# Kernel optimization log

Hardware: AMD Instinct MI355X
Metric: run time of the kernel (lower is better)

## Reference

```python
import jax, jax.numpy as jnp
import numpy as np

B, K, NPER, Fin, Fmem, H = 64, 16, 256, 256, 128, 8
LN_EPS = 1e-5


def _build_edges():
    # each memory slot (src) attends over all K slots + NPER nodes of its batch elem
    BK = B * K
    dest_chunks = []
    for b in range(B):
        dest_b = np.concatenate([b * K + np.arange(K), BK + b * NPER + np.arange(NPER)])
        dest_chunks.append(np.tile(dest_b, K))
    dest = np.concatenate(dest_chunks).astype(np.int32)
    src = np.repeat(np.arange(BK), K + NPER).astype(np.int32)
    return src, dest


def setup_inputs() -> dict:
    key = jax.random.key(0)
    ks = jax.random.split(key, 16)
    N = B * NPER
    BK = B * K
    src, dest = _build_edges()
    s = 0.02
    return {
        'x': jax.random.normal(ks[0], (N, Fin), jnp.float32),
        'memory': jax.random.normal(ks[1], (BK, Fmem), jnp.float32),
        'Wp': jax.random.normal(ks[2], (Fin, Fmem), jnp.float32) * s,
        'bp': jnp.zeros((Fmem,), jnp.float32),
        'Wqkv': jax.random.normal(ks[3], (Fmem, 3 * Fmem), jnp.float32) * s,  # bias=False
        'ln1_g': jnp.ones((Fmem,), jnp.float32),
        'ln1_b': jnp.zeros((Fmem,), jnp.float32),
        'W1': jax.random.normal(ks[4], (Fmem, Fmem), jnp.float32) * s,
        'b1': jnp.zeros((Fmem,), jnp.float32),
        'W2': jax.random.normal(ks[5], (Fmem, Fmem), jnp.float32) * s,
        'b2': jnp.zeros((Fmem,), jnp.float32),
        'ln2_g': jnp.ones((Fmem,), jnp.float32),
        'ln2_b': jnp.zeros((Fmem,), jnp.float32),
        'Wg': jax.random.normal(ks[6], (2 * Fmem, 2 * Fmem), jnp.float32) * s,
        'bg': jnp.zeros((2 * Fmem,), jnp.float32),
        'src': jnp.asarray(src),
        'dest': jnp.asarray(dest),
    }


def layer_norm(x, g, b):
    mu = x.mean(-1, keepdims=True)
    var = ((x - mu) ** 2).mean(-1, keepdims=True)
    return (x - mu) * jax.lax.rsqrt(var + LN_EPS) * g + b


def reference(x, memory, Wp, bp, Wqkv, ln1_g, ln1_b, W1, b1, W2, b2,
              ln2_g, ln2_b, Wg, bg, src, dest):
    BK, F = memory.shape
    Fh = F // H
    # input projection and concat [memory; x]
    xp = x @ Wp + bp                               # [N, Fmem]
    mem_cat = jnp.concatenate([memory, xp], 0)     # [BK + N, Fmem]
    # qkv projection (no bias), Fqk = Fv = Fmem
    q, k, v = jnp.split(mem_cat @ Wqkv, 3, axis=-1)
    q = (q * (float(Fh) ** -0.5)).reshape(-1, H, Fh)
    k = k.reshape(-1, H, Fh)
    v = v.reshape(-1, H, Fh)
    # per-edge attention scores
    aw = jnp.einsum('ehf,ehf->eh', q[src], k[dest])          # [E, H]
    # scatter softmax over src segments
    m = jax.ops.segment_max(aw, src, num_segments=BK)
    e = jnp.exp(aw - m[src])
    z = jax.ops.segment_sum(e, src, num_segments=BK)
    p = e / z[src]                                            # [E, H]
    # weighted scatter-sum aggregation
    out = jax.ops.segment_sum(p[:, :, None] * v[dest], src, num_segments=BK)
    out = out.reshape(BK, F)
    # residual + LN, MLP, residual + LN
    mem_tmp = layer_norm(memory + out, ln1_g, ln1_b)
    mem_update = jax.nn.relu(mem_tmp @ W1 + b1) @ W2 + b2
    mem_update = layer_norm(mem_tmp + mem_update, ln2_g, ln2_b)
    # feature-level LSTM-style gating
    gate = jnp.concatenate([memory, mem_update], -1) @ Wg + bg
    f, i = jnp.split(gate, 2, axis=-1)
    new_mem = memory * jax.nn.sigmoid(f) + mem_update * jax.nn.sigmoid(i)
    return new_mem  # original returns (output, memory) with output is memory
```

## Files before the change

kernel.cpp:

```cpp
#include <hip/hip_runtime.h>
#include <hip/hip_bf16.h>

#define B_    64
#define K_    16
#define NPER_ 256
#define FIN_  256
#define F_    128
#define H_    8
#define N_    (B_ * NPER_)
#define BK_   (B_ * K_)
#define KV_   (K_ + NPER_)
#define LN_EPS_ 1e-5f

typedef short short8v __attribute__((ext_vector_type(8)));
typedef float float4v __attribute__((ext_vector_type(4)));

__device__ __forceinline__ float bf2f(unsigned short u) {
    union { unsigned u; float f; } c; c.u = ((unsigned)u) << 16; return c.f;
}
template<bool BF>
__device__ __forceinline__ float ldT(const void* p, long i) {
    if (BF) return bf2f(((const unsigned short*)p)[i]);
    else    return ((const float*)p)[i];
}
template<bool BF>
__device__ __forceinline__ float2 ld2T(const void* p, long i) {
    if (BF) {
        const unsigned u = *(const unsigned*)((const unsigned short*)p + i);
        return make_float2(bf2f((unsigned short)(u & 0xffffu)),
                           bf2f((unsigned short)(u >> 16)));
    } else {
        return *(const float2*)((const float*)p + i);
    }
}
template<bool BF>
__device__ __forceinline__ float4 ld4T(const void* p, long i) {
    if (BF) {
        const uint2 u = *(const uint2*)((const unsigned short*)p + i);
        return make_float4(bf2f((unsigned short)(u.x & 0xffffu)),
                           bf2f((unsigned short)(u.x >> 16)),
                           bf2f((unsigned short)(u.y & 0xffffu)),
                           bf2f((unsigned short)(u.y >> 16)));
    } else {
        return *(const float4*)((const float*)p + i);
    }
}
template<bool BF>
__device__ __forceinline__ void stT(void* p, long i, float v) {
    if (BF) ((__hip_bfloat16*)p)[i] = __float2bfloat16(v);
    else    ((float*)p)[i] = v;
}
__device__ __forceinline__ bool is_bf(const unsigned* probe) {
    return probe[0] != 0x3F800000u;
}

__device__ __forceinline__ unsigned short f2bf_rne(float f) {
    union { float f; unsigned u; } c; c.f = f;
    const unsigned r = c.u + 0x7FFFu + ((c.u >> 16) & 1u);
    return (unsigned short)(r >> 16);
}
__device__ __forceinline__ unsigned long long pack4(unsigned short a, unsigned short b,
                                                    unsigned short c, unsigned short d) {
    return (unsigned long long)a | ((unsigned long long)b << 16)
         | ((unsigned long long)c << 32) | ((unsigned long long)d << 48);
}

#define LDK 40

template<bool BF>
__device__ void gemm_xp_body(const void* x, const void* Wp, const void* bp,
                             float* xp, short* Ah, short* Al, short* Bh, short* Bl) {
    const int t = threadIdx.x;
    const int row0 = blockIdx.x * 32;
    const int wave = t >> 6, lane = t & 63;
    const int wm = wave >> 1, wn = wave & 1;
    const int l15 = lane & 15, l4 = lane >> 4;
    float4v acc[4];
    #pragma unroll
    for (int fc = 0; fc < 4; ++fc) acc[fc] = (float4v){0.f, 0.f, 0.f, 0.f};

    for (int ks = 0; ks < 8; ++ks) {
        const int k0 = ks * 32;
        {
            const int ar = t >> 3, kq = (t & 7) * 4;
            const float4 v4 = ld4T<BF>(x, (long)(row0 + ar) * FIN_ + k0 + kq);
            unsigned short h0 = f2bf_rne(v4.x), h1 = f2bf_rne(v4.y);
            unsigned short h2 = f2bf_rne(v4.z), h3 = f2bf_rne(v4.w);
            *(unsigned long long*)(Ah + ar * LDK + kq) = pack4(h0, h1, h2, h3);
            *(unsigned long long*)(Al + ar * LDK + kq) = pack4(
                f2bf_rne(v4.x - bf2f(h0)), f2bf_rne(v4.y - bf2f(h1)),
                f2bf_rne(v4.z - bf2f(h2)), f2bf_rne(v4.w - bf2f(h3)));
        }
        {
            const int j = t & 127, khh = (t >> 7) * 16;
            unsigned short hh[16], ll[16];
            #pragma unroll
            for (int kk = 0; kk < 16; ++kk) {
                const float w = ldT<BF>(Wp, (long)(k0 + khh + kk) * F_ + j);
                hh[kk] = f2bf_rne(w);
                ll[kk] = f2bf_rne(w - bf2f(hh[kk]));
            }
            #pragma unroll
            for (int g = 0; g < 4; ++g) {
                *(unsigned long long*)(Bh + j * LDK + khh + 4 * g) =
                    pack4(hh[4*g], hh[4*g+1], hh[4*g+2], hh[4*g+3]);
                *(unsigned long long*)(Bl + j * LDK + khh + 4 * g) =
                    pack4(ll[4*g], ll[4*g+1], ll[4*g+2], ll[4*g+3]);
            }
        }
        __syncthreads();
        {
            const int abase = (wm * 16 + l15) * LDK + 8 * l4;
            const short8v ah = *(const short8v*)(Ah + abase);
            const short8v al = *(const short8v*)(Al + abase);
            #pragma unroll
            for (int fc = 0; fc < 4; ++fc) {
                const int bbase = (wn * 64 + fc * 16 + l15) * LDK + 8 * l4;
                const short8v bh = *(const short8v*)(Bh + bbase);
                const short8v bl = *(const short8v*)(Bl + bbase);
                acc[fc] = __builtin_amdgcn_mfma_f32_16x16x32_bf16(ah, bh, acc[fc], 0, 0, 0);
                acc[fc] = __builtin_amdgcn_mfma_f32_16x16x32_bf16(ah, bl, acc[fc], 0, 0, 0);
                acc[fc] = __builtin_amdgcn_mfma_f32_16x16x32_bf16(al, bh, acc[fc], 0, 0, 0);
            }
        }
        __syncthreads();
    }
    #pragma unroll
    for (int fc = 0; fc < 4; ++fc) {
        const int col = wn * 64 + fc * 16 + l15;
        const float bb = ldT<BF>(bp, col);
        #pragma unroll
        for (int reg = 0; reg < 4; ++reg) {
            const int row = row0 + wm * 16 + l4 * 4 + reg;
            xp[(long)row * F_ + col] = acc[fc][reg] + bb;
        }
    }
}
__global__ __launch_bounds__(256) void k_gemm_xp(const void* x, const void* Wp,
        const void* bp, const unsigned* probe, float* xp) {
    __shared__ __align__(16) short Ah[32 * LDK];
    __shared__ __align__(16) short Al[32 * LDK];
    __shared__ __align__(16) short Bh[128 * LDK];
    __shared__ __align__(16) short Bl[128 * LDK];
    if (is_bf(probe)) gemm_xp_body<true >(x, Wp, bp, xp, Ah, Al, Bh, Bl);
    else              gemm_xp_body<false>(x, Wp, bp, xp, Ah, Al, Bh, Bl);
}

template<bool BF>
__device__ void gemm_qkv_body(const float* xp, const void* mem, const void* Wqkv,
                              float* kx, float* vx, float* qm, float* km, float* vm,
                              short* Ah, short* Al, short* Bh, short* Bl) {
    const int mb = blockIdx.x, nb = blockIdx.y;
    const bool isMem = (mb >= 512);
    const int t = threadIdx.x;
    const int wave = t >> 6, lane = t & 63;
    const int wm = wave >> 1, wn = wave & 1;
    const int l15 = lane & 15, l4 = lane >> 4;
    float4v acc[4];
    #pragma unroll
    for (int fc = 0; fc < 4; ++fc) acc[fc] = (float4v){0.f, 0.f, 0.f, 0.f};

    for (int ks = 0; ks < 4; ++ks) {
        const int k0 = ks * 32;
        {
            const int ar = t >> 3, kq = (t & 7) * 4;
            float4 v4;
            if (isMem) v4 = ld4T<BF>(mem, (long)((mb - 512) * 32 + ar) * F_ + k0 + kq);
            else       v4 = *(const float4*)(xp + (long)(mb * 32 + ar) * F_ + k0 + kq);
            unsigned short h0 = f2bf_rne(v4.x), h1 = f2bf_rne(v4.y);
            unsigned short h2 = f2bf_rne(v4.z), h3 = f2bf_rne(v4.w);
            *(unsigned long long*)(Ah + ar * LDK + kq) = pack4(h0, h1, h2, h3);
            *(unsigned long long*)(Al + ar * LDK + kq) = pack4(
                f2bf_rne(v4.x - bf2f(h0)), f2bf_rne(v4.y - bf2f(h1)),
                f2bf_rne(v4.z - bf2f(h2)), f2bf_rne(v4.w - bf2f(h3)));
        }
        {
            const int j = t & 127, khh = (t >> 7) * 16;
            unsigned short hh[16], ll[16];
            #pragma unroll
            for (int kk = 0; kk < 16; ++kk) {
                const float w = ldT<BF>(Wqkv, (long)(k0 + khh + kk) * 384 + nb * 128 + j);
                hh[kk] = f2bf_rne(w);
                ll[kk] = f2bf_rne(w - bf2f(hh[kk]));
            }
            #pragma unroll
            for (int g = 0; g < 4; ++g) {
                *(unsigned long long*)(Bh + j * LDK + khh + 4 * g) =
                    pack4(hh[4*g], hh[4*g+1], hh[4*g+2], hh[4*g+3]);
                *(unsigned long long*)(Bl + j * LDK + khh + 4 * g) =
                    pack4(ll[4*g], ll[4*g+1], ll[4*g+2], ll[4*g+3]);
            }
        }
        __syncthreads();
        {
            const int abase = (wm * 16 + l15) * LDK + 8 * l4;
            const short8v ah = *(const short8v*)(Ah + abase);
            const short8v al = *(const short8v*)(Al + abase);
            #pragma unroll
            for (int fc = 0; fc < 4; ++fc) {
                const int bbase = (wn * 64 + fc * 16 + l15) * LDK + 8 * l4;
                const short8v bh = *(const short8v*)(Bh + bbase);
                const short8v bl = *(const short8v*)(Bl + bbase);
                acc[fc] = __builtin_amdgcn_mfma_f32_16x16x32_bf16(ah, bh, acc[fc], 0, 0, 0);
                acc[fc] = __builtin_amdgcn_mfma_f32_16x16x32_bf16(ah, bl, acc[fc], 0, 0, 0);
                acc[fc] = __builtin_amdgcn_mfma_f32_16x16x32_bf16(al, bh, acc[fc], 0, 0, 0);
            }
        }
        __syncthreads();
    }
    #pragma unroll
    for (int fc = 0; fc < 4; ++fc) {
        const int col = wn * 64 + fc * 16 + l15;
        #pragma unroll
        for (int reg = 0; reg < 4; ++reg) {
            const int mrow = mb * 32 + wm * 16 + l4 * 4 + reg;
            const float v = acc[fc][reg];
            if (!isMem) {
                ((nb == 1) ? kx : vx)[(long)mrow * F_ + col] = v;
            } else {
                const long s = mrow - 16384;
                if      (nb == 0) qm[s * F_ + col] = v * 0.25f;
                else if (nb == 1) km[s * F_ + col] = v;
                else              vm[s * F_ + col] = v;
            }
        }
    }
}
__global__ __launch_bounds__(256) void k_gemm_qkv(const float* xp, const void* mem,
        const void* Wqkv, const unsigned* probe,
        float* kx, float* vx, float* qm, float* km, float* vm) {
    if (blockIdx.y == 0 && blockIdx.x < 512) return;
    __shared__ __align__(16) short Ah[32 * LDK];
    __shared__ __align__(16) short Al[32 * LDK];
    __shared__ __align__(16) short Bh[128 * LDK];
    __shared__ __align__(16) short Bl[128 * LDK];
    if (is_bf(probe)) gemm_qkv_body<true >(xp, mem, Wqkv, kx, vx, qm, km, vm, Ah, Al, Bh, Bl);
    else              gemm_qkv_body<false>(xp, mem, Wqkv, kx, vx, qm, km, vm, Ah, Al, Bh, Bl);
}

#define KPAD 20
__global__ __launch_bounds__(256) void k_attn(const float* qm, const float* km,
        const float* vm, const float* kx, const float* vx, float* attn_out) {
    __shared__ float qh[16 * 16];
    __shared__ float kh[KV_ * KPAD];
    __shared__ float vh[KV_ * KPAD];
    __shared__ float S[16 * KV_];
    const int b = blockIdx.x >> 3, h = blockIdx.x & 7;
    const int t = threadIdx.x;
    qh[t] = qm[(long)(b * 16 + (t >> 4)) * F_ + h * 16 + (t & 15)];
    if (t < 64) {
        const int e = t >> 2, d4 = (t & 3) * 4;
        const long a = (long)(b * K_ + e) * F_ + h * 16 + d4;
        *(float4*)(kh + e * KPAD + d4) = *(const float4*)(km + a);
        *(float4*)(vh + e * KPAD + d4) = *(const float4*)(vm + a);
    }
    #pragma unroll
    for (int p = 0; p < 4; ++p) {
        const int i = t + p * 256;
        const int e = i >> 2, d4 = (i & 3) * 4;
        const long a = ((long)(b * NPER_) + e) * F_ + h * 16 + d4;
        *(float4*)(kh + (16 + e) * KPAD + d4) = *(const float4*)(kx + a);
        *(float4*)(vh + (16 + e) * KPAD + d4) = *(const float4*)(vx + a);
    }
    __syncthreads();
    {
        const int e = t;
        float acc[16];
        #pragma unroll
        for (int r = 0; r < 16; ++r) acc[r] = 0.f;
        #pragma unroll
        for (int dq = 0; dq < 16; dq += 4) {
            const float4 k4 = *(const float4*)(kh + e * KPAD + dq);
            #pragma unroll
            for (int r = 0; r < 16; ++r) {
                const float4 q4 = *(const float4*)(qh + r * 16 + dq);
                acc[r] += q4.x * k4.x + q4.y * k4.y + q4.z * k4.z + q4.w * k4.w;
            }
        }
        #pragma unroll
        for (int r = 0; r < 16; ++r) S[r * KV_ + e] = acc[r];
        const int e2 = 256 + (t >> 4), r2 = t & 15;
        float a2 = 0.f;
        #pragma unroll
        for (int dq = 0; dq < 16; dq += 4) {
            const float4 k4 = *(const float4*)(kh + e2 * KPAD + dq);
            const float4 q4 = *(const float4*)(qh + r2 * 16 + dq);
            a2 += q4.x * k4.x + q4.y * k4.y + q4.z * k4.z + q4.w * k4.w;
        }
        S[r2 * KV_ + e2] = a2;
    }
    __syncthreads();
    {
        const int wave = t >> 6, lane = t & 63;
        for (int r = wave; r < 16; r += 4) {
            float m = -1e30f;
            for (int e = lane; e < KV_; e += 64) m = fmaxf(m, S[r * KV_ + e]);
            for (int off = 32; off; off >>= 1) m = fmaxf(m, __shfl_xor(m, off));
            float z = 0.f;
            for (int e = lane; e < KV_; e += 64) {
                const float p = __expf(S[r * KV_ + e] - m);
                S[r * KV_ + e] = p; z += p;
            }
            for (int off = 32; off; off >>= 1) z += __shfl_xor(z, off);
            const float inv = 1.f / z;
            for (int e = lane; e < KV_; e += 64) S[r * KV_ + e] *= inv;
        }
    }
    __syncthreads();
    {
        const int r = t >> 4, d = t & 15;
        float o0 = 0.f, o1 = 0.f, o2 = 0.f, o3 = 0.f;
        for (int e = 0; e < KV_; e += 4) {
            const float4 p4 = *(const float4*)(S + r * KV_ + e);
            o0 += p4.x * vh[(e + 0) * KPAD + d];
            o1 += p4.y * vh[(e + 1) * KPAD + d];
            o2 += p4.z * vh[(e + 2) * KPAD + d];
            o3 += p4.w * vh[(e + 3) * KPAD + d];
        }
        attn_out[((long)(b * 16) + r) * F_ + h * 16 + d] = (o0 + o1) + (o2 + o3);
    }
}

#define R4 2
template<bool BF>
__device__ void post_body(const void* mem, const float* attn,
                          const void* ln1g, const void* ln1b,
                          const void* W1, const void* b1,
                          const void* W2, const void* b2,
                          const void* ln2g, const void* ln2b,
                          const void* Wg, const void* bg,
                          void* out,
                          float* ms, float* hs, float* ts, float* cat,
                          float* gs, float (*pb)[R4][256]) {
    const int t = threadIdx.x;
    const int r0b = blockIdx.x * R4;
    if (t < 128) {
        const int rr = t >> 6, c0 = (t & 63) * 2;
        const long gbase = (long)(r0b + rr) * F_ + c0;
        const float mv0 = ldT<BF>(mem, gbase), mv1 = ldT<BF>(mem, gbase + 1);
        const float2 a2 = *(const float2*)(attn + gbase);
        const float y0 = mv0 + a2.x, y1 = mv1 + a2.y;
        float s = y0 + y1;
        #pragma unroll
        for (int off = 32; off; off >>= 1) s += __shfl_xor(s, off);
        const float mu = s * (1.f / 128.f);
        const float d0 = y0 - mu, d1 = y1 - mu;
        float v = d0 * d0 + d1 * d1;
        #pragma unroll
        for (int off = 32; off; off >>= 1) v += __shfl_xor(v, off);
        const float inv = rsqrtf(v * (1.f / 128.f) + LN_EPS_);
        ms[rr * F_ + c0]     = d0 * inv * ldT<BF>(ln1g, c0)     + ldT<BF>(ln1b, c0);
        ms[rr * F_ + c0 + 1] = d1 * inv * ldT<BF>(ln1g, c0 + 1) + ldT<BF>(ln1b, c0 + 1);
        cat[rr * 256 + c0]     = mv0;
        cat[rr * 256 + c0 + 1] = mv1;
    }
    __syncthreads();
    {
        const int jp2 = (t & 63) * 2, r = (t >> 6) & 1, kh = t >> 7;
        const float* mr = ms + r * F_ + kh * 64;
        float a0 = 0.f, a1 = 0.f, b0v = 0.f, b1v = 0.f;
        #pragma unroll 4
        for (int f = 0; f < 64; f += 4) {
            const float4 m4 = *(const float4*)(mr + f);
            const float2 w0 = ld2T<BF>(W1, (long)(kh * 64 + f + 0) * F_ + jp2);
            const float2 w1 = ld2T<BF>(W1, (long)(kh * 64 + f + 1) * F_ + jp2);
            const float2 w2 = ld2T<BF>(W1, (long)(kh * 64 + f + 2) * F_ + jp2);
            const float2 w3 = ld2T<BF>(W1, (long)(kh * 64 + f + 3) * F_ + jp2);
            a0  += m4.x * w0.x + m4.z * w2.x;
            a1  += m4.y * w1.x + m4.w * w3.x;
            b0v += m4.x * w0.y + m4.z * w2.y;
            b1v += m4.y * w1.y + m4.w * w3.y;
        }
        pb[kh][r][jp2]     = a0 + a1;
        pb[kh][r][jp2 + 1] = b0v + b1v;
    }
    __syncthreads();
    {
        const int r = t >> 7, c = t & 127;
        hs[r * F_ + c] = fmaxf(pb[0][r][c] + pb[1][r][c] + ldT<BF>(b1, c), 0.f);
    }
    __syncthreads();
    {
        const int jp2 = (t & 63) * 2, r = (t >> 6) & 1, kh = t >> 7;
        const float* hr = hs + r * F_ + kh * 64;
        float a0 = 0.f, a1 = 0.f, b0v = 0.f, b1v = 0.f;
        #pragma unroll 4
        for (int f = 0; f < 64; f += 4) {
            const float4 h4 = *(const float4*)(hr + f);
            const float2 w0 = ld2T<BF>(W2, (long)(kh * 64 + f + 0) * F_ + jp2);
            const float2 w1 = ld2T<BF>(W2, (long)(kh * 64 + f + 1) * F_ + jp2);
            const float2 w2 = ld2T<BF>(W2, (long)(kh * 64 + f + 2) * F_ + jp2);
            const float2 w3 = ld2T<BF>(W2, (long)(kh * 64 + f + 3) * F_ + jp2);
            a0  += h4.x * w0.x + h4.z * w2.x;
            a1  += h4.y * w1.x + h4.w * w3.x;
            b0v += h4.x * w0.y + h4.z * w2.y;
            b1v += h4.y * w1.y + h4.w * w3.y;
        }
        pb[kh][r][jp2]     = a0 + a1;
        pb[kh][r][jp2 + 1] = b0v + b1v;
    }
    __syncthreads();
    {
        const int r = t >> 7, c = t & 127;
        ts[r * F_ + c] = ms[r * F_ + c] + pb[0][r][c] + pb[1][r][c] + ldT<BF>(b2, c);
    }
    __syncthreads();
    if (t < 128) {
        const int rr = t >> 6, c0 = (t & 63) * 2;
        const float z0 = ts[rr * F_ + c0], z1 = ts[rr * F_ + c0 + 1];
        float s = z0 + z1;
        #pragma unroll
        for (int off = 32; off; off >>= 1) s += __shfl_xor(s, off);
        const float mu = s * (1.f / 128.f);
        const float d0 = z0 - mu, d1 = z1 - mu;
        float v = d0 * d0 + d1 * d1;
        #pragma unroll
        for (int off = 32; off; off >>= 1) v += __shfl_xor(v, off);
        const float inv = rsqrtf(v * (1.f / 128.f) + LN_EPS_);
        cat[rr * 256 + 128 + c0]     = d0 * inv * ldT<BF>(ln2g, c0)     + ldT<BF>(ln2b, c0);
        cat[rr * 256 + 128 + c0 + 1] = d1 * inv * ldT<BF>(ln2g, c0 + 1) + ldT<BF>(ln2b, c0 + 1);
    }
    __syncthreads();
    {
        const int cq4 = (t & 63) * 4, r = (t >> 6) & 1, kh = t >> 7;
        const float* cr = cat + r * 256 + kh * 128;
        float a0 = 0.f, a1 = 0.f, a2 = 0.f, a3 = 0.f;
        #pragma unroll 2
        for (int f = 0; f < 128; f += 4) {
            const float4 c4 = *(const float4*)(cr + f);
            float4 w;
            w = ld4T<BF>(Wg, (long)(kh * 128 + f + 0) * 256 + cq4);
            a0 += c4.x * w.x; a1 += c4.x * w.y; a2 += c4.x * w.z; a3 += c4.x * w.w;
            w = ld4T<BF>(Wg, (long)(kh * 128 + f + 1) * 256 + cq4);
            a0 += c4.y * w.x; a1 += c4.y * w.y; a2 += c4.y * w.z; a3 += c4.y * w.w;
            w = ld4T<BF>(Wg, (long)(kh * 128 + f + 2) * 256 + cq4);
            a0 += c4.z * w.x; a1 += c4.z * w.y; a2 += c4.z * w.z; a3 += c4.z * w.w;
            w = ld4T<BF>(Wg, (long)(kh * 128 + f + 3) * 256 + cq4);
            a0 += c4.w * w.x; a1 += c4.w * w.y; a2 += c4.w * w.z; a3 += c4.w * w.w;
        }
        pb[kh][r][cq4 + 0] = a0; pb[kh][r][cq4 + 1] = a1;
        pb[kh][r][cq4 + 2] = a2; pb[kh][r][cq4 + 3] = a3;
    }
    __syncthreads();
    {
        #pragma unroll
        for (int o = t; o < 512; o += 256) {
            const int r = o >> 8, c = o & 255;
            gs[r * 256 + c] = pb[0][r][c] + pb[1][r][c] + ldT<BF>(bg, c);
        }
    }
    __syncthreads();
    {
        const int r = t >> 7, cf = t & 127;
        const float gf = gs[r * 256 + cf], gi = gs[r * 256 + 128 + cf];
        const float m0 = cat[r * 256 + cf], uu = cat[r * 256 + 128 + cf];
        const float val = m0 * (1.f / (1.f + __expf(-gf)))
                        + uu * (1.f / (1.f + __expf(-gi)));
        stT<BF>(out, (long)(r0b + r) * F_ + cf, val);
    }
}
__global__ __launch_bounds__(256) void k_post(const void* mem, const float* attn,
        const void* ln1g, const void* ln1b, const void* W1, const void* b1,
        const void* W2, const void* b2, const void* ln2g, const void* ln2b,
        const void* Wg, const void* bg, const unsigned* probe, void* out) {
    __shared__ float ms[R4 * F_];
    __shared__ float hs[R4 * F_];
    __shared__ float ts[R4 * F_];
    __shared__ float cat[R4 * 2 * F_];
    __shared__ float gs[R4 * 2 * F_];
    __shared__ float pb[2][R4][256];
    if (is_bf(probe)) post_body<true >(mem, attn, ln1g, ln1b, W1, b1, W2, b2,
                                       ln2g, ln2b, Wg, bg, out, ms, hs, ts, cat, gs, pb);
    else              post_body<false>(mem, attn, ln1g, ln1b, W1, b1, W2, b2,
                                       ln2g, ln2b, Wg, bg, out, ms, hs, ts, cat, gs, pb);
}

extern "C" void kernel_launch(void* const* d_in, const int* in_sizes, int n_in,
                              void* d_out, int out_size, void* d_ws, size_t ws_size,
                              hipStream_t stream) {
    const void* x      = d_in[0];
    const void* memory = d_in[1];
    const void* Wp     = d_in[2];
    const void* bp     = d_in[3];
    const void* Wqkv   = d_in[4];
    const void* ln1g   = d_in[5];
    const void* ln1b   = d_in[6];
    const void* W1     = d_in[7];
    const void* b1     = d_in[8];
    const void* W2     = d_in[9];
    const void* b2     = d_in[10];
    const void* ln2g   = d_in[11];
    const void* ln2b   = d_in[12];
    const void* Wg     = d_in[13];
    const void* bg     = d_in[14];
    const unsigned* probe = (const unsigned*)d_in[5];

    float* ws   = (float*)d_ws;
    float* xp   = ws;
    float* kx   = xp + (long)N_ * F_;
    float* vx   = kx + (long)N_ * F_;
    float* qm   = vx + (long)N_ * F_;
    float* km   = qm + (long)BK_ * F_;
    float* vm   = km + (long)BK_ * F_;
    float* attn = vm + (long)BK_ * F_;

    k_gemm_xp  <<<N_ / 32, 256, 0, stream>>>(x, Wp, bp, probe, xp);
    k_gemm_qkv <<<dim3((N_ + BK_) / 32, 3), 256, 0, stream>>>(xp, memory, Wqkv, probe,
                                                              kx, vx, qm, km, vm);
    k_attn     <<<B_ * H_, 256, 0, stream>>>(qm, km, vm, kx, vx, attn);
    k_post     <<<BK_ / R4, 256, 0, stream>>>(memory, attn, ln1g, ln1b, W1, b1,
                                              W2, b2, ln2g, ln2b, Wg, bg, probe, d_out);
}
```

Measured before the change: 155.0 us.

## Fuse input projection and QKV GEMMs into one kernel keeping xp in LDS

Merges the x@Wp projection and the K/V projection of the node rows into one kernel. The projected tile stays in shared memory as a split bf16 hi/lo pair and is never written to global memory. Memory rows compute Q, K and V in the same launch. When inputs are bf16, the hi/lo split and the extra MFMAs are dropped for already-bf16 operands. This removes a launch and the xp global round trip, at the cost of larger LDS use (60KB) and lower occupancy per block.

```diff
diff --git a/kernel.cpp b/kernel.cpp
--- a/kernel.cpp
+++ b/kernel.cpp
@@ -66,176 +66,250 @@
 }
 
 #define LDK 40
+#define CH  (32 * LDK)
 
 template<bool BF>
-__device__ void gemm_xp_body(const void* x, const void* Wp, const void* bp,
-                             float* xp, short* Ah, short* Al, short* Bh, short* Bl) {
+__device__ void proj_body(const void* x, const void* mem, const void* Wp,
+                          const void* bp, const void* Wqkv,
+                          float* kx, float* vx, float* qm, float* km, float* vm,
+                          short* pool) {
     const int t = threadIdx.x;
-    const int row0 = blockIdx.x * 32;
+    const int mb = blockIdx.x;
     const int wave = t >> 6, lane = t & 63;
     const int wm = wave >> 1, wn = wave & 1;
     const int l15 = lane & 15, l4 = lane >> 4;
-    float4v acc[4];
-    #pragma unroll
-    for (int fc = 0; fc < 4; ++fc) acc[fc] = (float4v){0.f, 0.f, 0.f, 0.f};
-
-    for (int ks = 0; ks < 8; ++ks) {
-        const int k0 = ks * 32;
+    short* A2h = pool;
+    short* A2l = pool + 5120;
+    short* Rb  = pool + 10240;
+
+    if (mb < 512) {
+        const long row0 = (long)mb * 32;
+        short* A1h = Rb;
+        short* A1l = Rb + 1280;
+        short* B1h = Rb + 2560;
+        short* B1l = Rb + 7680;
+        float4v acc1[4];
+        #pragma unroll
+        for (int fc = 0; fc < 4; ++fc) acc1[fc] = (float4v){0.f, 0.f, 0.f, 0.f};
+        for (int ks = 0; ks < 8; ++ks) {
+            const int k0 = ks * 32;
+            {
+                const int ar = t >> 3, kq = (t & 7) * 4;
+                const long idx = (row0 + ar) * FIN_ + k0 + kq;
+                if (BF) {
+                    const uint2 u = *(const uint2*)((const unsigned short*)x + idx);
+                    *(uint2*)(A1h + ar * LDK + kq) = u;
+                } else {
+                    const float4 v4 = *(const float4*)((const float*)x + idx);
+                    unsigned short h0 = f2bf_rne(v4.x), h1 = f2bf_rne(v4.y);
+                    unsigned short h2 = f2bf_rne(v4.z), h3 = f2bf_rne(v4.w);
+                    *(unsigned long long*)(A1h + ar * LDK + kq) = pack4(h0, h1, h2, h3);
+                    *(unsigned long long*)(A1l + ar * LDK + kq) = pack4(
+                        f2bf_rne(v4.x - bf2f(h0)), f2bf_rne(v4.y - bf2f(h1)),
+                        f2bf_rne(v4.z - bf2f(h2)), f2bf_rne(v4.w - bf2f(h3)));
+                }
+            }
+            {
+                const int j = t & 127, kh0 = (t >> 7) * 16;
+                #pragma unroll
+                for (int q = 0; q < 4; ++q) {
+                    if (BF) {
+                        const unsigned short* w = (const unsigned short*)Wp;
+                        const long r = (long)(k0 + kh0 + 4 * q) * F_ + j;
+                        *(unsigned long long*)(B1h + j * LDK + kh0 + 4 * q) =
+                            pack4(w[r], w[r + F_], w[r + 2 * F_], w[r + 3 * F_]);
+                    } else {
+                        const float* w = (const float*)Wp;
+                        const long r = (long)(k0 + kh0 + 4 * q) * F_ + j;
+                        const float w0 = w[r], w1 = w[r + F_], w2 = w[r + 2 * F_], w3 = w[r + 3 * F_];
+                        unsigned short h0 = f2bf_rne(w0), h1 = f2bf_rne(w1);
+                        unsigned short h2 = f2bf_rne(w2), h3 = f2bf_rne(w3);
+                        *(unsigned long long*)(B1h + j * LDK + kh0 + 4 * q) = pack4(h0, h1, h2, h3);
+                        *(unsigned long long*)(B1l + j * LDK + kh0 + 4 * q) = pack4(
+                            f2bf_rne(w0 - bf2f(h0)), f2bf_rne(w1 - bf2f(h1)),
+                            f2bf_rne(w2 - bf2f(h2)), f2bf_rne(w3 - bf2f(h3)));
+                    }
+                }
+            }
+            __syncthreads();
+            {
+                const int ab = (wm * 16 + l15) * LDK + 8 * l4;
+                const short8v ah = *(const short8v*)(A1h + ab);
+                short8v al;
+                if (!BF) al = *(const short8v*)(A1l + ab);
+                #pragma unroll
+                for (int fc = 0; fc < 4; ++fc) {
+                    const int bb = (wn * 64 + fc * 16 + l15) * LDK + 8 * l4;
+                    const short8v bh = *(const short8v*)(B1h + bb);
+                    acc1[fc] = __builtin_amdgcn_mfma_f32_16x16x32_bf16(ah, bh, acc1[fc], 0, 0, 0);
+                    if (!BF) {
+                        const short8v bl = *(const short8v*)(B1l + bb);
+                        acc1[fc] = __builtin_amdgcn_mfma_f32_16x16x32_bf16(ah, bl, acc1[fc], 0, 0, 0);
+                        acc1[fc] = __builtin_amdgcn_mfma_f32_16x16x32_bf16(al, bh, acc1[fc], 0, 0, 0);
+                    }
+                }
+            }
+            __syncthreads();
+        }
+        #pragma unroll
+        for (int fc = 0; fc < 4; ++fc) {
+            const int col = wn * 64 + fc * 16 + l15;
+            const int c = col >> 5, kk = col & 31;
+            const float bb = ldT<BF>(bp, col);
+            #pragma unroll
+            for (int reg = 0; reg < 4; ++reg) {
+                const int row = wm * 16 + l4 * 4 + reg;
+                const float v = acc1[fc][reg] + bb;
+                const unsigned short h = f2bf_rne(v);
+                A2h[c * CH + row * LDK + kk] = (short)h;
+                A2l[c * CH + row * LDK + kk] = (short)f2bf_rne(v - bf2f(h));
+            }
+        }
+        short* B2h = Rb;
+        short* B2l = Rb + 10240;
+        float4v acc2[8];
+        #pragma unroll
+        for (int fc = 0; fc < 8; ++fc) acc2[fc] = (float4v){0.f, 0.f, 0.f, 0.f};
+        for (int c2 = 0; c2 < 4; ++c2) {
+            __syncthreads();
+            {
+                const int jj = t;
+                #pragma unroll
+                for (int q = 0; q < 8; ++q) {
+                    const long r = (long)(c2 * 32 + 4 * q) * 384 + 128 + jj;
+                    if (BF) {
+                        const unsigned short* w = (const unsigned short*)Wqkv;
+                        *(unsigned long long*)(B2h + jj * LDK + 4 * q) =
+                            pack4(w[r], w[r + 384], w[r + 768], w[r + 1152]);
+                    } else {
+                        const float* w = (const float*)Wqkv;
+                        const float w0 = w[r], w1 = w[r + 384], w2 = w[r + 768], w3 = w[r + 1152];
+                        unsigned short h0 = f2bf_rne(w0), h1 = f2bf_rne(w1);
+                        unsigned short h2 = f2bf_rne(w2), h3 = f2bf_rne(w3);
+                        *(unsigned long long*)(B2h + jj * LDK + 4 * q) = pack4(h0, h1, h2, h3);
+                        *(unsigned long long*)(B2l + jj * LDK + 4 * q) = pack4(
+                            f2bf_rne(w0 - bf2f(h0)), f2bf_rne(w1 - bf2f(h1)),
+                            f2bf_rne(w2 - bf2f(h2)), f2bf_rne(w3 - bf2f(h3)));
+                    }
+                }
+            }
+            __syncthreads();
+            {
+                const int ab = c2 * CH + (wm * 16 + l15) * LDK + 8 * l4;
+                const short8v a2h = *(const short8v*)(A2h + ab);
+                const short8v a2l = *(const short8v*)(A2l + ab);
+                #pragma unroll
+                for (int fc = 0; fc < 8; ++fc) {
+                    const int bb = (wn * 128 + fc * 16 + l15) * LDK + 8 * l4;
+                    const short8v bh = *(const short8v*)(B2h + bb);
+                    acc2[fc] = __builtin_amdgcn_mfma_f32_16x16x32_bf16(a2h, bh, acc2[fc], 0, 0, 0);
+                    acc2[fc] = __builtin_amdgcn_mfma_f32_16x16x32_bf16(a2l, bh, acc2[fc], 0, 0, 0);
+                    if (!BF) {
+                        const short8v bl = *(const short8v*)(B2l + bb);
+                        acc2[fc] = __builtin_amdgcn_mfma_f32_16x16x32_bf16(a2h, bl, acc2[fc], 0, 0, 0);
+                    }
+                }
+            }
+        }
+        float* dst = wn ? vx : kx;
+        #pragma unroll
+        for (int fc = 0; fc < 8; ++fc) {
+            const int col = fc * 16 + l15;
+            #pragma unroll
+            for (int reg = 0; reg < 4; ++reg) {
+                const long row = row0 + wm * 16 + l4 * 4 + reg;
+                dst[row * F_ + col] = acc2[fc][reg];
+            }
+        }
+    } else {
+        const long srow0 = (long)(mb - 512) * 32;
+        short* Bgh = Rb;
+        short* Bgl = Rb + 5120;
         {
             const int ar = t >> 3, kq = (t & 7) * 4;
-            const float4 v4 = ld4T<BF>(x, (long)(row0 + ar) * FIN_ + k0 + kq);
-            unsigned short h0 = f2bf_rne(v4.x), h1 = f2bf_rne(v4.y);
-            unsigned short h2 = f2bf_rne(v4.z), h3 = f2bf_rne(v4.w);
-            *(unsigned long long*)(Ah + ar * LDK + kq) = pack4(h0, h1, h2, h3);
-            *(unsigned long long*)(Al + ar * LDK + kq) = pack4(
-                f2bf_rne(v4.x - bf2f(h0)), f2bf_rne(v4.y - bf2f(h1)),
-                f2bf_rne(v4.z - bf2f(h2)), f2bf_rne(v4.w - bf2f(h3)));
-        }
-        {
-            const int j = t & 127, khh = (t >> 7) * 16;
-            unsigned short hh[16], ll[16];
             #pragma unroll
-            for (int kk = 0; kk < 16; ++kk) {
-                const float w = ldT<BF>(Wp, (long)(k0 + khh + kk) * F_ + j);
-                hh[kk] = f2bf_rne(w);
-                ll[kk] = f2bf_rne(w - bf2f(hh[kk]));
-            }
+            for (int c = 0; c < 4; ++c) {
+                const long idx = (srow0 + ar) * F_ + c * 32 + kq;
+                if (BF) {
+                    const uint2 u = *(const uint2*)((const unsigned short*)mem + idx);
+                    *(uint2*)(A2h + c * CH + ar * LDK + kq) = u;
+                } else {
+                    const float4 v4 = *(const float4*)((const float*)mem + idx);
+                    unsigned short h0 = f2bf_rne(v4.x), h1 = f2bf_rne(v4.y);
+                    unsigned short h2 = f2bf_rne(v4.z), h3 = f2bf_rne(v4.w);
+                    *(unsigned long long*)(A2h + c * CH + ar * LDK + kq) = pack4(h0, h1, h2, h3);
+                    *(unsigned long long*)(A2l + c * CH + ar * LDK + kq) = pack4(
+                        f2bf_rne(v4.x - bf2f(h0)), f2bf_rne(v4.y - bf2f(h1)),
+                        f2bf_rne(v4.z - bf2f(h2)), f2bf_rne(v4.w - bf2f(h3)));
+                }
+            }
+        }
+        for (int g = 0; g < 3; ++g) {
+            float4v accg[4];
             #pragma unroll
-            for (int g = 0; g < 4; ++g) {
-                *(unsigned long long*)(Bh + j * LDK + khh + 4 * g) =
-                    pack4(hh[4*g], hh[4*g+1], hh[4*g+2], hh[4*g+3]);
-                *(unsigned long long*)(Bl + j * LDK + khh + 4 * g) =
-                    pack4(ll[4*g], ll[4*g+1], ll[4*g+2], ll[4*g+3]);
-            }
-        }
-        __syncthreads();
-        {
-            const int abase = (wm * 16 + l15) * LDK + 8 * l4;
-            const short8v ah = *(const short8v*)(Ah + abase);
-            const short8v al = *(const short8v*)(Al + abase);
+            for (int fc = 0; fc < 4; ++fc) accg[fc] = (float4v){0.f, 0.f, 0.f, 0.f};
+            for (int c2 = 0; c2 < 4; ++c2) {
+                __syncthreads();
+                {
+                    const int j = t & 127, kh0 = (t >> 7) * 16;
+                    #pragma unroll
+                    for (int q = 0; q < 4; ++q) {
+                        const long r = (long)(c2 * 32 + kh0 + 4 * q) * 384 + g * 128 + j;
+                        if (BF) {
+                            const unsigned short* w = (const unsigned short*)Wqkv;
+                            *(unsigned long long*)(Bgh + j * LDK + kh0 + 4 * q) =
+                                pack4(w[r], w[r + 384], w[r + 768], w[r + 1152]);
+                        } else {
+                            const float* w = (const float*)Wqkv;
+                            const float w0 = w[r], w1 = w[r + 384], w2 = w[r + 768], w3 = w[r + 1152];
+                            unsigned short h0 = f2bf_rne(w0), h1 = f2bf_rne(w1);
+                            unsigned short h2 = f2bf_rne(w2), h3 = f2bf_rne(w3);
+                            *(unsigned long long*)(Bgh + j * LDK + kh0 + 4 * q) = pack4(h0, h1, h2, h3);
+                            *(unsigned long long*)(Bgl + j * LDK + kh0 + 4 * q) = pack4(
+                                f2bf_rne(w0 - bf2f(h0)), f2bf_rne(w1 - bf2f(h1)),
+                                f2bf_rne(w2 - bf2f(h2)), f2bf_rne(w3 - bf2f(h3)));
+                        }
+                    }
+                }
+                __syncthreads();
+                {
+                    const int ab = c2 * CH + (wm * 16 + l15) * LDK + 8 * l4;
+                    const short8v ah = *(const short8v*)(A2h + ab);
+                    short8v al;
+                    if (!BF) al = *(const short8v*)(A2l + ab);
+                    #pragma unroll
+                    for (int fc = 0; fc < 4; ++fc) {
+                        const int bb = (wn * 64 + fc * 16 + l15) * LDK + 8 * l4;
+                        const short8v bh = *(const short8v*)(Bgh + bb);
+                        accg[fc] = __builtin_amdgcn_mfma_f32_16x16x32_bf16(ah, bh, accg[fc], 0, 0, 0);
+                        if (!BF) {
+                            const short8v bl = *(const short8v*)(Bgl + bb);
+                            accg[fc] = __builtin_amdgcn_mfma_f32_16x16x32_bf16(ah, bl, accg[fc], 0, 0, 0);
+                            accg[fc] = __builtin_amdgcn_mfma_f32_16x16x32_bf16(al, bh, accg[fc], 0, 0, 0);
+                        }
+                    }
+                }
+            }
+            float* dst = (g == 0) ? qm : ((g == 1) ? km : vm);
+            const float sc = (g == 0) ? 0.25f : 1.f;
             #pragma unroll
             for (int fc = 0; fc < 4; ++fc) {
-                const int bbase = (wn * 64 + fc * 16 + l15) * LDK + 8 * l4;
-                const short8v bh = *(const short8v*)(Bh + bbase);
-                const short8v bl = *(const short8v*)(Bl + bbase);
-                acc[fc] = __builtin_amdgcn_mfma_f32_16x16x32_bf16(ah, bh, acc[fc], 0, 0, 0);
-                acc[fc] = __builtin_amdgcn_mfma_f32_16x16x32_bf16(ah, bl, acc[fc], 0, 0, 0);
-                acc[fc] = __builtin_amdgcn_mfma_f32_16x16x32_bf16(al, bh, acc[fc], 0, 0, 0);
-            }
-        }
-        __syncthreads();
-    }
-    #pragma unroll
-    for (int fc = 0; fc < 4; ++fc) {
-        const int col = wn * 64 + fc * 16 + l15;
-        const float bb = ldT<BF>(bp, col);
-        #pragma unroll
-        for (int reg = 0; reg < 4; ++reg) {
-            const int row = row0 + wm * 16 + l4 * 4 + reg;
-            xp[(long)row * F_ + col] = acc[fc][reg] + bb;
-        }
-    }
-}
-__global__ __launch_bounds__(256) void k_gemm_xp(const void* x, const void* Wp,
-        const void* bp, const unsigned* probe, float* xp) {
-    __shared__ __align__(16) short Ah[32 * LDK];
-    __shared__ __align__(16) short Al[32 * LDK];
-    __shared__ __align__(16) short Bh[128 * LDK];
-    __shared__ __align__(16) short Bl[128 * LDK];
-    if (is_bf(probe)) gemm_xp_body<true >(x, Wp, bp, xp, Ah, Al, Bh, Bl);
-    else              gemm_xp_body<false>(x, Wp, bp, xp, Ah, Al, Bh, Bl);
-}
-
-template<bool BF>
-__device__ void gemm_qkv_body(const float* xp, const void* mem, const void* Wqkv,
-                              float* kx, float* vx, float* qm, float* km, float* vm,
-                              short* Ah, short* Al, short* Bh, short* Bl) {
-    const int mb = blockIdx.x, nb = blockIdx.y;
-    const bool isMem = (mb >= 512);
-    const int t = threadIdx.x;
-    const int wave = t >> 6, lane = t & 63;
-    const int wm = wave >> 1, wn = wave & 1;
-    const int l15 = lane & 15, l4 = lane >> 4;
-    float4v acc[4];
-    #pragma unroll
-    for (int fc = 0; fc < 4; ++fc) acc[fc] = (float4v){0.f, 0.f, 0.f, 0.f};
-
-    for (int ks = 0; ks < 4; ++ks) {
-        const int k0 = ks * 32;
-        {
-            const int ar = t >> 3, kq = (t & 7) * 4;
-            float4 v4;
-            if (isMem) v4 = ld4T<BF>(mem, (long)((mb - 512) * 32 + ar) * F_ + k0 + kq);
-            else       v4 = *(const float4*)(xp + (long)(mb * 32 + ar) * F_ + k0 + kq);
-            unsigned short h0 = f2bf_rne(v4.x), h1 = f2bf_rne(v4.y);
-            unsigned short h2 = f2bf_rne(v4.z), h3 = f2bf_rne(v4.w);
-            *(unsigned long long*)(Ah + ar * LDK + kq) = pack4(h0, h1, h2, h3);
-            *(unsigned long long*)(Al + ar * LDK + kq) = pack4(
-                f2bf_rne(v4.x - bf2f(h0)), f2bf_rne(v4.y - bf2f(h1)),
-                f2bf_rne(v4.z - bf2f(h2)), f2bf_rne(v4.w - bf2f(h3)));
-        }
-        {
-            const int j = t & 127, khh = (t >> 7) * 16;
-            unsigned short hh[16], ll[16];
-            #pragma unroll
-            for (int kk = 0; kk < 16; ++kk) {
-                const float w = ldT<BF>(Wqkv, (long)(k0 + khh + kk) * 384 + nb * 128 + j);
-                hh[kk] = f2bf_rne(w);
-                ll[kk] = f2bf_rne(w - bf2f(hh[kk]));
-            }
-            #pragma unroll
-            for (int g = 0; g < 4; ++g) {
-                *(unsigned long long*)(Bh + j * LDK + khh + 4 * g) =
-                    pack4(hh[4*g], hh[4*g+1], hh[4*g+2], hh[4*g+3]);
-                *(unsigned long long*)(Bl + j * LDK + khh + 4 * g) =
-                    pack4(ll[4*g], ll[4*g+1], ll[4*g+2], ll[4*g+3]);
-            }
-        }
-        __syncthreads();
-        {
-            const int abase = (wm * 16 + l15) * LDK + 8 * l4;
-            const short8v ah = *(const short8v*)(Ah + abase);
-            const short8v al = *(const short8v*)(Al + abase);
-            #pragma unroll
-            for (int fc = 0; fc < 4; ++fc) {
-                const int bbase = (wn * 64 + fc * 16 + l15) * LDK + 8 * l4;
-                const short8v bh = *(const short8v*)(Bh + bbase);
-                const short8v bl = *(const short8v*)(Bl + bbase);
-                acc[fc] = __builtin_amdgcn_mfma_f32_16x16x32_bf16(ah, bh, acc[fc], 0, 0, 0);
-                acc[fc] = __builtin_amdgcn_mfma_f32_16x16x32_bf16(ah, bl, acc[fc], 0, 0, 0);
-                acc[fc] = __builtin_amdgcn_mfma_f32_16x16x32_bf16(al, bh, acc[fc], 0, 0, 0);
-            }
-        }
-        __syncthreads();
-    }
-    #pragma unroll
-    for (int fc = 0; fc < 4; ++fc) {
-        const int col = wn * 64 + fc * 16 + l15;
-        #pragma unroll
-        for (int reg = 0; reg < 4; ++reg) {
-            const int mrow = mb * 32 + wm * 16 + l4 * 4 + reg;
-            const float v = acc[fc][reg];
-            if (!isMem) {
-                ((nb == 1) ? kx : vx)[(long)mrow * F_ + col] = v;
-            } else {
-                const long s = mrow - 16384;
-                if      (nb == 0) qm[s * F_ + col] = v * 0.25f;
-                else if (nb == 1) km[s * F_ + col] = v;
-                else              vm[s * F_ + col] = v;
-            }
-        }
-    }
-}
-__global__ __launch_bounds__(256) void k_gemm_qkv(const float* xp, const void* mem,
-        const void* Wqkv, const unsigned* probe,
+                const int col = wn * 64 + fc * 16 + l15;
+                #pragma unroll
+                for (int reg = 0; reg < 4; ++reg) {
+                    const long row = srow0 + wm * 16 + l4 * 4 + reg;
+                    dst[row * F_ + col] = accg[fc][reg] * sc;
+                }
+            }
+        }
+    }
+}
+__global__ __launch_bounds__(256) void k_proj(const void* x, const void* mem,
+        const void* Wp, const void* bp, const void* Wqkv, const unsigned* probe,
         float* kx, float* vx, float* qm, float* km, float* vm) {
-    if (blockIdx.y == 0 && blockIdx.x < 512) return;
-    __shared__ __align__(16) short Ah[32 * LDK];
-    __shared__ __align__(16) short Al[32 * LDK];
-    __shared__ __align__(16) short Bh[128 * LDK];
-    __shared__ __align__(16) short Bl[128 * LDK];
-    if (is_bf(probe)) gemm_qkv_body<true >(xp, mem, Wqkv, kx, vx, qm, km, vm, Ah, Al, Bh, Bl);
-    else              gemm_qkv_body<false>(xp, mem, Wqkv, kx, vx, qm, km, vm, Ah, Al, Bh, Bl);
+    __shared__ __align__(16) short pool[30720];
+    if (is_bf(probe)) proj_body<true >(x, mem, Wp, bp, Wqkv, kx, vx, qm, km, vm, pool);
+    else              proj_body<false>(x, mem, Wp, bp, Wqkv, kx, vx, qm, km, vm, pool);
 }
 
 #define KPAD 20
@@ -496,18 +570,16 @@
     const unsigned* probe = (const unsigned*)d_in[5];
 
     float* ws   = (float*)d_ws;
-    float* xp   = ws;
-    float* kx   = xp + (long)N_ * F_;
+    float* kx   = ws;
     float* vx   = kx + (long)N_ * F_;
     float* qm   = vx + (long)N_ * F_;
     float* km   = qm + (long)BK_ * F_;
     float* vm   = km + (long)BK_ * F_;
     float* attn = vm + (long)BK_ * F_;
 
-    k_gemm_xp  <<<N_ / 32, 256, 0, stream>>>(x, Wp, bp, probe, xp);
-    k_gemm_qkv <<<dim3((N_ + BK_) / 32, 3), 256, 0, stream>>>(xp, memory, Wqkv, probe,
-                                                              kx, vx, qm, km, vm);
-    k_attn     <<<B_ * H_, 256, 0, stream>>>(qm, km, vm, kx, vx, attn);
-    k_post     <<<BK_ / R4, 256, 0, stream>>>(memory, attn, ln1g, ln1b, W1, b1,
-                                              W2, b2, ln2g, ln2b, Wg, bg, probe, d_out);
-}
+    k_proj <<<544, 256, 0, stream>>>(x, memory, Wp, bp, Wqkv, probe,
+                                     kx, vx, qm, km, vm);
+    k_attn <<<B_ * H_, 256, 0, stream>>>(qm, km, vm, kx, vx, attn);
+    k_post <<<BK_ / R4, 256, 0, stream>>>(memory, attn, ln1g, ln1b, W1, b1,
+                                          W2, b2, ln2g, ln2b, Wg, bg, probe, d_out);
+}
```

Result: no change. 154.6 us (-0.2%).
